# Optimization experiments

Hardware: AMD Instinct MI355X
Metric: run time of the kernel (lower is better)

Reference implementation:

```python
import jax, jax.numpy as jnp
import numpy as np

N_NODES = 100000
N_EDGES = 1_600_000
F_IN, HID, N_CLS = 128, 64, 32
NEG_SLOPE = 0.2  # PyG GATv2Conv default


def _segment_softmax(scores, seg, num_segments):
    # numerically stable softmax over edges grouped by destination node
    m = jax.ops.segment_max(scores, seg, num_segments=num_segments)
    ex = jnp.exp(scores - m[seg])
    s = jax.ops.segment_sum(ex, seg, num_segments=num_segments)
    return ex / (s[seg] + 1e-16)


def _gatv2_layer(x, src, dst, Wl, bl, Wr, br, att, bias, num_nodes):
    xl = x @ Wl + bl              # source transform  [N, C]
    xr = x @ Wr + br              # target transform  [N, C]
    # per-edge GATv2 attention logit: a . leaky_relu(xl_j + xr_i)
    e = jax.nn.leaky_relu(xl[src] + xr[dst], NEG_SLOPE) @ att  # [E]
    alpha = _segment_softmax(e, dst, num_nodes)                 # [E]
    out = jax.ops.segment_sum(alpha[:, None] * xl[src], dst, num_segments=num_nodes)
    return out + bias


def _add_self_loops(edge_index, n):
    loops = jnp.arange(n, dtype=edge_index.dtype)
    return jnp.concatenate([edge_index, jnp.stack([loops, loops])], axis=1)


def setup_inputs() -> dict:
    key = jax.random.key(0)
    ks = jax.random.split(key, 8)
    s1 = 1.0 / np.sqrt(F_IN)
    s2 = 1.0 / np.sqrt(HID)
    return {
        "x": jax.random.normal(ks[0], (N_NODES, F_IN), jnp.float32),
        "edge_index": jax.random.randint(ks[1], (2, N_EDGES), 0, N_NODES, jnp.int64),
        "W1l": jax.random.normal(ks[2], (F_IN, HID), jnp.float32) * s1,
        "b1l": jnp.zeros((HID,), jnp.float32),
        "W1r": jax.random.normal(ks[3], (F_IN, HID), jnp.float32) * s1,
        "b1r": jnp.zeros((HID,), jnp.float32),
        "att1": jax.random.normal(ks[4], (HID,), jnp.float32) * s2,
        "bias1": jnp.zeros((HID,), jnp.float32),
        "W2l": jax.random.normal(ks[5], (HID, N_CLS), jnp.float32) * s2,
        "b2l": jnp.zeros((N_CLS,), jnp.float32),
        "W2r": jax.random.normal(ks[6], (HID, N_CLS), jnp.float32) * s2,
        "b2r": jnp.zeros((N_CLS,), jnp.float32),
        "att2": jax.random.normal(ks[7], (N_CLS,), jnp.float32) / np.sqrt(N_CLS),
        "bias2": jnp.zeros((N_CLS,), jnp.float32),
    }


def reference(x, edge_index, W1l, b1l, W1r, b1r, att1, bias1,
              W2l, b2l, W2r, b2r, att2, bias2):
    n = x.shape[0]
    ei = _add_self_loops(edge_index, n)
    src, dst = ei[0], ei[1]
    h = jax.nn.relu(_gatv2_layer(x, src, dst, W1l, b1l, W1r, b1r, att1, bias1, n))
    # F.dropout(training=False) is identity in eval mode
    out = _gatv2_layer(h, src, dst, W2l, b2l, W2r, b2r, att2, bias2, n)
    return out
```

## Files before the change

### kernel.cpp

```cpp
#include <hip/hip_runtime.h>
#include <hip/hip_fp16.h>
#include <math.h>

#define F_IN 128
#define HID 64
#define NCLS 32
#define NEG 0.2f
#define NBKT 256
#define CHUNK 8192

using bf8 = __attribute__((ext_vector_type(8))) short;
using f4v = __attribute__((ext_vector_type(4))) float;
typedef _Float16 hv2 __attribute__((ext_vector_type(2)));

__device__ __forceinline__ void f4fma(float4& a, float s, const float4& w) {
    a.x = fmaf(s, w.x, a.x);
    a.y = fmaf(s, w.y, a.y);
    a.z = fmaf(s, w.z, a.z);
    a.w = fmaf(s, w.w, a.w);
}
__device__ __forceinline__ unsigned short f2bf(float f) {
    unsigned u = __float_as_uint(f);
    return (unsigned short)((u + 0x7FFFu + ((u >> 16) & 1u)) >> 16);
}
__device__ __forceinline__ unsigned short f2h(float f) {
    return __half_as_ushort(__float2half(f));
}
__device__ __forceinline__ float h2f(unsigned short u) {
    return __half2float(__ushort_as_half(u));
}
__device__ __forceinline__ unsigned pkaddabs(unsigned a, unsigned b) {
    hv2 r = __builtin_bit_cast(hv2, a) + __builtin_bit_cast(hv2, b);
    return __builtin_bit_cast(unsigned, r) & 0x7FFF7FFFu;
}
__device__ __forceinline__ float fdot2(unsigned a, unsigned b, float c) {
    return __builtin_amdgcn_fdot2(__builtin_bit_cast(hv2, a),
                                  __builtin_bit_cast(hv2, b), c, false);
}
__device__ __forceinline__ float h2lo(unsigned a) {
    return (float)__builtin_bit_cast(hv2, a).x;
}
__device__ __forceinline__ float h2hi(unsigned a) {
    return (float)__builtin_bit_cast(hv2, a).y;
}
template <int CTRL>
__device__ __forceinline__ float dpp_add(float v) {
    int t = __builtin_amdgcn_update_dpp(0, __float_as_int(v), CTRL, 0xf, 0xf, true);
    return v + __int_as_float(t);
}
__device__ __forceinline__ float swz16_add(float v) {
    int t = __builtin_amdgcn_ds_swizzle(__float_as_int(v), 0x401F);
    return v + __int_as_float(t);
}


__global__ __launch_bounds__(256) void zeroBuckets(int* __restrict__ bucketSize, int BK) {
    int i = blockIdx.x * 256 + threadIdx.x;
    if (i < BK) bucketSize[i] = 0;
}

__global__ __launch_bounds__(256) void bucketHist(const int* __restrict__ ei,
                                                  int Eorig, int Etot,
                                                  int* __restrict__ bucketSize, int BK) {
    __shared__ int h[512];
    int t = threadIdx.x;
    for (int j = t; j < BK; j += 256) h[j] = 0;
    __syncthreads();
    int base = blockIdx.x * CHUNK;
    int end = base + CHUNK < Etot ? base + CHUNK : Etot;
    for (int i = base + t; i < end; i += 256) {
        int dst = i < Eorig ? ei[Eorig + i] : i - Eorig;
        atomicAdd(&h[dst >> 8], 1);
    }
    __syncthreads();
    for (int j = t; j < BK; j += 256)
        if (h[j]) atomicAdd(&bucketSize[j], h[j]);
}

__global__ __launch_bounds__(256) void bucketScan(const int* __restrict__ bucketSize,
                                                  int* __restrict__ bucketStart,
                                                  int* __restrict__ bucketCursor,
                                                  int BK, int Etot) {
    __shared__ int sd[256];
    int t = threadIdx.x;
    int v0 = (2 * t     < BK) ? bucketSize[2 * t]     : 0;
    int v1 = (2 * t + 1 < BK) ? bucketSize[2 * t + 1] : 0;
    int ts = v0 + v1;
    sd[t] = ts;
    __syncthreads();
    for (int off = 1; off < 256; off <<= 1) {
        int x = (t >= off) ? sd[t - off] : 0;
        __syncthreads();
        sd[t] += x;
        __syncthreads();
    }
    int excl = sd[t] - ts;
    if (2 * t < BK)     { bucketStart[2 * t] = excl;          bucketCursor[2 * t] = excl; }
    if (2 * t + 1 < BK) { bucketStart[2 * t + 1] = excl + v0; bucketCursor[2 * t + 1] = excl + v0; }
    if (t == 255) bucketStart[BK] = Etot;
}

__global__ __launch_bounds__(256) void bucketScatter(const int* __restrict__ ei,
                                                     int Eorig, int Etot,
                                                     int* __restrict__ bucketCursor,
                                                     int* __restrict__ pairs, int BK) {
    __shared__ int h[512], lbase[512], hcur[512];
    int t = threadIdx.x;
    for (int j = t; j < BK; j += 256) { h[j] = 0; hcur[j] = 0; }
    __syncthreads();
    int base = blockIdx.x * CHUNK;
    int end = base + CHUNK < Etot ? base + CHUNK : Etot;
    for (int i = base + t; i < end; i += 256) {
        int dst = i < Eorig ? ei[Eorig + i] : i - Eorig;
        atomicAdd(&h[dst >> 8], 1);
    }
    __syncthreads();
    for (int j = t; j < BK; j += 256)
        lbase[j] = h[j] ? atomicAdd(&bucketCursor[j], h[j]) : 0;
    __syncthreads();
    for (int i = base + t; i < end; i += 256) {
        int src, dst;
        if (i < Eorig) { src = ei[i]; dst = ei[Eorig + i]; }
        else           { src = dst = i - Eorig; }
        int b = dst >> 8;
        int off = atomicAdd(&hcur[b], 1);
        pairs[lbase[b] + off] = (src << 8) | (dst & 255);
    }
}

__global__ __launch_bounds__(256) void bucketCSR(const int* __restrict__ pairs,
                                                 const int* __restrict__ bucketStart,
                                                 int* __restrict__ rowstart,
                                                 int* __restrict__ cnt,
                                                 int* __restrict__ srclist, int N) {
    __shared__ int c[256], cur[256];
    int t = threadIdx.x;
    int b = blockIdx.x;
    int lo = b * NBKT;
    int eb = bucketStart[b], ee = bucketStart[b + 1];
    c[t] = 0;
    __syncthreads();
    for (int i = eb + t; i < ee; i += 256)
        atomicAdd(&c[pairs[i] & 255], 1);
    __syncthreads();
    cur[t] = c[t];
    __syncthreads();
    for (int off = 1; off < 256; off <<= 1) {
        int x = (t >= off) ? cur[t - off] : 0;
        __syncthreads();
        cur[t] += x;
        __syncthreads();
    }
    int excl = cur[t] - c[t];
    int node = lo + t;
    if (node < N) { rowstart[node] = eb + excl; cnt[node] = c[t]; }
    __syncthreads();
    cur[t] = excl;
    __syncthreads();
    for (int i = eb + t; i < ee; i += 256) {
        int v = pairs[i];
        int pos = atomicAdd(&cur[v & 255], 1);
        srclist[eb + pos] = v >> 8;
    }
}

__global__ __launch_bounds__(256) void prepW(const float* __restrict__ Wl,
                                             const float* __restrict__ Wr,
                                             const float* __restrict__ att1,
                                             const float* __restrict__ att2,
                                             uint4* __restrict__ wfrag,
                                             unsigned short* __restrict__ att1h,
                                             unsigned short* __restrict__ att2h) {
    int e = blockIdx.x * 256 + threadIdx.x;
    if (e >= 2048) {
        int i = e - 2048;
        if (i < HID) att1h[i] = f2h(att1[i]);
        else if (i < HID + NCLS) att2h[i - HID] = f2h(att2[i - HID]);
        return;
    }
    int lane = e & 63;
    int kt = (e >> 6) & 3;
    int ct = (e >> 8) & 3;
    int mat = e >> 10;
    const float* W = mat ? Wr : Wl;
    int k0 = kt * 32 + (lane >> 4) * 8;
    int c = ct * 16 + (lane & 15);
    unsigned short h[8];
#pragma unroll
    for (int j = 0; j < 8; j++) h[j] = f2bf(W[(k0 + j) * HID + c]);
    wfrag[e] = *(uint4*)h;
}

__global__ __launch_bounds__(256) void transform1(const float* __restrict__ x,
                                                  const uint4* __restrict__ wfrag,
                                                  const float* __restrict__ bl,
                                                  const float* __restrict__ br,
                                                  const float* __restrict__ att,
                                                  unsigned short* __restrict__ xlh,
                                                  unsigned short* __restrict__ xrh,
                                                  float* __restrict__ sl, int N) {
    __shared__ uint4 sw[2048];
    int t = threadIdx.x;
#pragma unroll
    for (int j = 0; j < 8; j++) sw[t + j * 256] = wfrag[t + j * 256];
    __syncthreads();

    int w = t >> 6, lane = t & 63;
    int nb = blockIdx.x * 64 + w * 16;
    int m = lane & 15, quad = lane >> 4;

    int arow = nb + m; if (arow >= N) arow = N - 1;
    const float* xrow = x + (size_t)arow * F_IN + quad * 8;
    bf8 afr[4];
#pragma unroll
    for (int kt = 0; kt < 4; kt++) {
        float4 lo = *(const float4*)(xrow + kt * 32);
        float4 hi = *(const float4*)(xrow + kt * 32 + 4);
        unsigned short hh[8];
        hh[0] = f2bf(lo.x); hh[1] = f2bf(lo.y); hh[2] = f2bf(lo.z); hh[3] = f2bf(lo.w);
        hh[4] = f2bf(hi.x); hh[5] = f2bf(hi.y); hh[6] = f2bf(hi.z); hh[7] = f2bf(hi.w);
        afr[kt] = *(bf8*)hh;
    }

    float am[4];
#pragma unroll
    for (int ct = 0; ct < 4; ct++) am[ct] = att[ct * 16 + m];
    float slp[4] = {0.f, 0.f, 0.f, 0.f};

#pragma unroll
    for (int mat = 0; mat < 2; mat++) {
        const float* bias = mat ? br : bl;
#pragma unroll
        for (int ct = 0; ct < 4; ct++) {
            f4v acc = {0.f, 0.f, 0.f, 0.f};
#pragma unroll
            for (int kt = 0; kt < 4; kt++) {
                bf8 bfr = *(bf8*)&sw[((mat * 4 + ct) * 4 + kt) * 64 + lane];
                acc = __builtin_amdgcn_mfma_f32_16x16x32_bf16(afr[kt], bfr, acc, 0, 0, 0);
            }
            int ch = ct * 16 + m;
            float bv = bias[ch];
#pragma unroll
            for (int reg = 0; reg < 4; reg++) {
                int node = nb + quad * 4 + reg;
                float o = acc[reg] + bv;
                if (mat) {
                    if (node < N) xrh[(size_t)node * HID + ch] = f2h(o);
                } else {
                    unsigned short hb = f2h(o);
                    slp[reg] = fmaf(am[ct], h2f(hb), slp[reg]);
                    if (node < N) xlh[(size_t)node * HID + ch] = hb;
                }
            }
        }
    }
#pragma unroll
    for (int o2 = 1; o2 < 16; o2 <<= 1) {
#pragma unroll
        for (int reg = 0; reg < 4; reg++) slp[reg] += __shfl_xor(slp[reg], o2, 64);
    }
    if (m == 0) {
#pragma unroll
        for (int reg = 0; reg < 4; reg++) {
            int node = nb + quad * 4 + reg;
            if (node < N) sl[node] = 0.6f * slp[reg];
        }
    }
}

__global__ __launch_bounds__(256) void transform2(const float* __restrict__ h,
                                                  const float* __restrict__ Wl,
                                                  const float* __restrict__ bl,
                                                  const float* __restrict__ Wr,
                                                  const float* __restrict__ br,
                                                  const float* __restrict__ att,
                                                  unsigned short* __restrict__ xlh,
                                                  unsigned short* __restrict__ xrh,
                                                  float* __restrict__ sl, int N) {
    __shared__ float sWl[HID * NCLS];
    __shared__ float sWr[HID * NCLS];
    __shared__ float sx[128][68];
    int t = threadIdx.x;
    int nb = blockIdx.x * 128;

#pragma unroll
    for (int j = 0; j < 2; j++) {
        int f = t + j * 256;
        ((float4*)sWl)[f] = ((const float4*)Wl)[f];
        ((float4*)sWr)[f] = ((const float4*)Wr)[f];
    }
    int maxf = (N - nb) * 16;
#pragma unroll
    for (int j = 0; j < 8; j++) {
        int f = t + j * 256;
        int node = f >> 4, kc = f & 15;
        float4 v = {0.f, 0.f, 0.f, 0.f};
        if (f < maxf) v = ((const float4*)(h + (size_t)nb * HID))[f];
        v.x = fmaxf(v.x, 0.f);
        v.y = fmaxf(v.y, 0.f);
        v.z = fmaxf(v.z, 0.f);
        v.w = fmaxf(v.w, 0.f);
        *(float4*)&sx[node][kc * 4] = v;
    }
    __syncthreads();

    int c4 = (t & 7) * 4;
    int slot = t >> 3;
    float4 bl4 = *(const float4*)(bl + c4);
    float4 br4 = *(const float4*)(br + c4);
    float4 at4 = *(const float4*)(att + c4);
    float4 accl[4] = {bl4, bl4, bl4, bl4};
    float4 accr[4] = {br4, br4, br4, br4};

#pragma unroll 4
    for (int k4 = 0; k4 < HID / 4; k4++) {
        int k = k4 * 4;
        float4 wl0 = *(const float4*)&sWl[(k + 0) * NCLS + c4];
        float4 wl1 = *(const float4*)&sWl[(k + 1) * NCLS + c4];
        float4 wl2 = *(const float4*)&sWl[(k + 2) * NCLS + c4];
        float4 wl3 = *(const float4*)&sWl[(k + 3) * NCLS + c4];
        float4 wr0 = *(const float4*)&sWr[(k + 0) * NCLS + c4];
        float4 wr1 = *(const float4*)&sWr[(k + 1) * NCLS + c4];
        float4 wr2 = *(const float4*)&sWr[(k + 2) * NCLS + c4];
        float4 wr3 = *(const float4*)&sWr[(k + 3) * NCLS + c4];
#pragma unroll
        for (int j = 0; j < 4; j++) {
            float4 xv = *(const float4*)&sx[slot + j * 32][k];
            f4fma(accl[j], xv.x, wl0); f4fma(accr[j], xv.x, wr0);
            f4fma(accl[j], xv.y, wl1); f4fma(accr[j], xv.y, wr1);
            f4fma(accl[j], xv.z, wl2); f4fma(accr[j], xv.z, wr2);
            f4fma(accl[j], xv.w, wl3); f4fma(accr[j], xv.w, wr3);
        }
    }
#pragma unroll
    for (int j = 0; j < 4; j++) {
        ushort4 o;
        o.x = f2h(accl[j].x); o.y = f2h(accl[j].y);
        o.z = f2h(accl[j].z); o.w = f2h(accl[j].w);
        ushort4 orr;
        orr.x = f2h(accr[j].x); orr.y = f2h(accr[j].y);
        orr.z = f2h(accr[j].z); orr.w = f2h(accr[j].w);
        float slpj = fmaf(at4.x, h2f(o.x),
                     fmaf(at4.y, h2f(o.y),
                     fmaf(at4.z, h2f(o.z), at4.w * h2f(o.w))));
        slpj += __shfl_xor(slpj, 1, 64);
        slpj += __shfl_xor(slpj, 2, 64);
        slpj += __shfl_xor(slpj, 4, 64);
        int g = nb + slot + j * 32;
        if (g < N) {
            *(ushort4*)(xlh + (size_t)g * NCLS + c4) = o;
            *(ushort4*)(xrh + (size_t)g * NCLS + c4) = orr;
            if ((t & 7) == 0) sl[g] = 0.6f * slpj;
        }
    }
}

#define AGG_BATCH(EIDX, CLAMP, WEXPR)                                 \
    {                                                                 \
        int eidx = row + (EIDX);                                      \
        if (CLAMP) eidx = min(eidx, rowend1);                         \
        int src = srclist[eidx];                                      \
        float tA = sl[src];                                           \
        unsigned vp[NH];                                              \
        const unsigned short* rowp = xlh + (unsigned)src * C + cb0;   \
        if (NH == 4) *(uint4*)vp = *(const uint4*)rowp;               \
        else         *(uint2*)vp = *(const uint2*)rowp;               \
        float pa = 0.f;                                               \
        _Pragma("unroll")                                             \
        for (int j = 0; j < NH; j++)                                  \
            pa = fdot2(pkaddabs(vp[j], xrp[j]), atp[j], pa);          \
        pa = dpp_add<0x128>(pa);                                      \
        pa = swz16_add(pa);                                           \
        pa += __shfl_xor(pa, 32, 64);                                 \
        float wgt = (WEXPR);                                          \
        s += wgt;                                                     \
        _Pragma("unroll")                                             \
        for (int j = 0; j < NH; j++) {                                \
            acc[2 * j]     = fmaf(wgt, h2lo(vp[j]), acc[2 * j]);      \
            acc[2 * j + 1] = fmaf(wgt, h2hi(vp[j]), acc[2 * j + 1]);  \
        }                                                             \
    }

template <int C>
__global__ __launch_bounds__(256) void fusedAggE(const unsigned short* __restrict__ xlh,
                                                 const unsigned short* __restrict__ xrh,
                                                 const unsigned short* __restrict__ atth,
                                                 const float* __restrict__ sl,
                                                 const int* __restrict__ rowstart,
                                                 const int* __restrict__ cnt,
                                                 const int* __restrict__ srclist,
                                                 const float* __restrict__ bias,
                                                 float* __restrict__ out, int N) {
    constexpr int CH = C / 8;
    constexpr int NH = CH / 2;
    int wid = threadIdx.x >> 6;
    int lane = threadIdx.x & 63;
    int n = blockIdx.x * 4 + wid;
    if (n >= N) return;

    int slot = lane & 7;
    int pos  = lane >> 3;
    int cb0  = pos * CH;

    unsigned xrp[NH], atp[NH];
    if (NH == 4) {
        *(uint4*)xrp = *(const uint4*)(xrh + (size_t)n * C + cb0);
        *(uint4*)atp = *(const uint4*)(atth + cb0);
    } else {
        *(uint2*)xrp = *(const uint2*)(xrh + (size_t)n * C + cb0);
        *(uint2*)atp = *(const uint2*)(atth + cb0);
    }

    int row = rowstart[n];
    int deg = cnt[n];
    int rowend1 = row + deg - 1;

    float s = 0.f;
    float acc[CH];
#pragma unroll
    for (int c = 0; c < CH; c++) acc[c] = 0.f;

    for (int cb = 0; cb < deg; cb += 64) {
        int len = deg - cb; if (len > 64) len = 64;
        int nfull = len >> 3, rem = len & 7;
#pragma unroll 2
        for (int b = 0; b < nfull; b++) {
            AGG_BATCH(cb + b * 8 + slot, false, __expf(fmaf(0.4f, pa, tA)))
        }
        if (rem) {
            AGG_BATCH(cb + nfull * 8 + slot, true,
                      (slot < rem) ? __expf(fmaf(0.4f, pa, tA)) : 0.f)
        }
    }
#pragma unroll
    for (int c = 0; c < CH; c++) {
        acc[c] = dpp_add<0xB1>(acc[c]);
        acc[c] = dpp_add<0x4E>(acc[c]);
        acc[c] = dpp_add<0x141>(acc[c]);
    }
    s = dpp_add<0xB1>(s);
    s = dpp_add<0x4E>(s);
    s = dpp_add<0x141>(s);

    if (slot == 0) {
        float inv = 1.f / (s + 1e-16f);
        float o8[CH];
        float bi[CH];
        if (NH == 4) {
            *(float4*)&bi[0] = *(const float4*)(bias + cb0);
            *(float4*)&bi[4] = *(const float4*)(bias + cb0 + 4);
        } else {
            *(float4*)&bi[0] = *(const float4*)(bias + cb0);
        }
#pragma unroll
        for (int c = 0; c < CH; c++) o8[c] = fmaf(acc[c], inv, bi[c]);
        if (NH == 4) {
            *(float4*)(out + (size_t)n * C + cb0)     = *(float4*)&o8[0];
            *(float4*)(out + (size_t)n * C + cb0 + 4) = *(float4*)&o8[4];
        } else {
            *(float4*)(out + (size_t)n * C + cb0) = *(float4*)&o8[0];
        }
    }
}

extern "C" void kernel_launch(void* const* d_in, const int* in_sizes, int n_in,
                              void* d_out, int out_size, void* d_ws, size_t ws_size,
                              hipStream_t stream) {
    const float* x     = (const float*)d_in[0];
    const int*   ei    = (const int*)d_in[1];
    const float* W1l   = (const float*)d_in[2];
    const float* b1l   = (const float*)d_in[3];
    const float* W1r   = (const float*)d_in[4];
    const float* b1r   = (const float*)d_in[5];
    const float* att1  = (const float*)d_in[6];
    const float* bias1 = (const float*)d_in[7];
    const float* W2l   = (const float*)d_in[8];
    const float* b2l   = (const float*)d_in[9];
    const float* W2r   = (const float*)d_in[10];
    const float* b2r   = (const float*)d_in[11];
    const float* att2  = (const float*)d_in[12];
    const float* bias2 = (const float*)d_in[13];
    float* out = (float*)d_out;

    int N     = in_sizes[0] / F_IN;
    int Eorig = in_sizes[1] / 2;
    int Etot  = Eorig + N;
    int BK    = (N + NBKT - 1) / NBKT;

    char* p = (char*)d_ws;
    auto alloc = [&](size_t bytes) { void* r = (void*)p; p += (bytes + 255) & ~(size_t)255; return r; };
    unsigned short* xl1h = (unsigned short*)alloc((size_t)N * HID * 2);
    unsigned short* xr1h = (unsigned short*)alloc((size_t)N * HID * 2);
    float* h       = (float*)alloc((size_t)N * HID * 4);
    unsigned short* xl2h = (unsigned short*)alloc((size_t)N * NCLS * 2);
    unsigned short* xr2h = (unsigned short*)alloc((size_t)N * NCLS * 2);
    int*   cnt     = (int*)alloc((size_t)N * 4);
    int*   rowstart= (int*)alloc((size_t)N * 4);
    int*   srclist = (int*)alloc((size_t)Etot * 4);
    uint4* wfrag   = (uint4*)alloc(2048 * 16);
    float* sl1     = (float*)alloc((size_t)N * 4);
    float* sl2     = (float*)alloc((size_t)N * 4);
    unsigned short* att1h = (unsigned short*)alloc(HID * 2);
    unsigned short* att2h = (unsigned short*)alloc(NCLS * 2);
    int*   bucketSize   = (int*)alloc(520 * 4);
    int*   bucketStart  = (int*)alloc(520 * 4);
    int*   bucketCursor = (int*)alloc(520 * 4);
    int*   pairs   = (int*)h;

    int nChunks = (Etot + CHUNK - 1) / CHUNK;

    zeroBuckets<<<2, 256, 0, stream>>>(bucketSize, BK);
    bucketHist<<<nChunks, 256, 0, stream>>>(ei, Eorig, Etot, bucketSize, BK);
    bucketScan<<<1, 256, 0, stream>>>(bucketSize, bucketStart, bucketCursor, BK, Etot);
    bucketScatter<<<nChunks, 256, 0, stream>>>(ei, Eorig, Etot, bucketCursor, pairs, BK);
    bucketCSR<<<BK, 256, 0, stream>>>(pairs, bucketStart, rowstart, cnt, srclist, N);

    prepW<<<9, 256, 0, stream>>>(W1l, W1r, att1, att2, wfrag, att1h, att2h);
    transform1<<<(N + 63) / 64, 256, 0, stream>>>(x, wfrag, b1l, b1r, att1, xl1h, xr1h, sl1, N);
    fusedAggE<HID><<<(N + 3) / 4, 256, 0, stream>>>(xl1h, xr1h, att1h, sl1, rowstart, cnt,
                                                    srclist, bias1, h, N);

    transform2<<<(N + 127) / 128, 256, 0, stream>>>(h, W2l, b2l, W2r, b2r, att2, xl2h, xr2h, sl2, N);
    fusedAggE<NCLS><<<(N + 3) / 4, 256, 0, stream>>>(xl2h, xr2h, att2h, sl2, rowstart, cnt,
                                                     srclist, bias2, out, N);
}
```

Baseline: 319.6 us.

## Cooperatively load edge indices per wave and software-pipeline row gathers in aggregation

The aggregation kernel now loads up to 64 source indices and their per-node scalars once per wave with one coalesced load, and hands them to slots via shuffles instead of each slot reloading them per batch. The gather of the next batch's xl row is issued before the current batch's dot product and accumulation, overlapping memory latency with compute. The swizzle reduction is replaced by a shuffle-xor, and the bucket zeroing kernel becomes a memset. This adds register pressure from the double-buffered rows and extra cross-lane shuffles.

```diff
diff --git a/kernel.cpp b/kernel.cpp
--- a/kernel.cpp
+++ b/kernel.cpp
@@ -48,16 +48,7 @@
     int t = __builtin_amdgcn_update_dpp(0, __float_as_int(v), CTRL, 0xf, 0xf, true);
     return v + __int_as_float(t);
 }
-__device__ __forceinline__ float swz16_add(float v) {
-    int t = __builtin_amdgcn_ds_swizzle(__float_as_int(v), 0x401F);
-    return v + __int_as_float(t);
-}
-
-
-__global__ __launch_bounds__(256) void zeroBuckets(int* __restrict__ bucketSize, int BK) {
-    int i = blockIdx.x * 256 + threadIdx.x;
-    if (i < BK) bucketSize[i] = 0;
-}
+
 
 __global__ __launch_bounds__(256) void bucketHist(const int* __restrict__ ei,
                                                   int Eorig, int Etot,
@@ -355,34 +346,15 @@
     }
 }
 
-#define AGG_BATCH(EIDX, CLAMP, WEXPR)                                 \
-    {                                                                 \
-        int eidx = row + (EIDX);                                      \
-        if (CLAMP) eidx = min(eidx, rowend1);                         \
-        int src = srclist[eidx];                                      \
-        float tA = sl[src];                                           \
-        unsigned vp[NH];                                              \
-        const unsigned short* rowp = xlh + (unsigned)src * C + cb0;   \
-        if (NH == 4) *(uint4*)vp = *(const uint4*)rowp;               \
-        else         *(uint2*)vp = *(const uint2*)rowp;               \
-        float pa = 0.f;                                               \
-        _Pragma("unroll")                                             \
-        for (int j = 0; j < NH; j++)                                  \
-            pa = fdot2(pkaddabs(vp[j], xrp[j]), atp[j], pa);          \
-        pa = dpp_add<0x128>(pa);                                      \
-        pa = swz16_add(pa);                                           \
-        pa += __shfl_xor(pa, 32, 64);                                 \
-        float wgt = (WEXPR);                                          \
-        s += wgt;                                                     \
-        _Pragma("unroll")                                             \
-        for (int j = 0; j < NH; j++) {                                \
-            acc[2 * j]     = fmaf(wgt, h2lo(vp[j]), acc[2 * j]);      \
-            acc[2 * j + 1] = fmaf(wgt, h2hi(vp[j]), acc[2 * j + 1]);  \
-        }                                                             \
+#define LOADROW(VP, SRC)                                                  \
+    {                                                                     \
+        const unsigned short* rp = xlh + (unsigned)(SRC) * C + cb0;       \
+        if (NH == 4) *(uint4*)(VP) = *(const uint4*)rp;                   \
+        else         *(uint2*)(VP) = *(const uint2*)rp;                   \
     }
 
 template <int C>
-__global__ __launch_bounds__(256) void fusedAggE(const unsigned short* __restrict__ xlh,
+__global__ __launch_bounds__(256) void fusedAggF(const unsigned short* __restrict__ xlh,
                                                  const unsigned short* __restrict__ xrh,
                                                  const unsigned short* __restrict__ atth,
                                                  const float* __restrict__ sl,
@@ -413,7 +385,6 @@
 
     int row = rowstart[n];
     int deg = cnt[n];
-    int rowend1 = row + deg - 1;
 
     float s = 0.f;
     float acc[CH];
@@ -422,14 +393,47 @@
 
     for (int cb = 0; cb < deg; cb += 64) {
         int len = deg - cb; if (len > 64) len = 64;
-        int nfull = len >> 3, rem = len & 7;
-#pragma unroll 2
-        for (int b = 0; b < nfull; b++) {
-            AGG_BATCH(cb + b * 8 + slot, false, __expf(fmaf(0.4f, pa, tA)))
-        }
-        if (rem) {
-            AGG_BATCH(cb + nfull * 8 + slot, true,
-                      (slot < rem) ? __expf(fmaf(0.4f, pa, tA)) : 0.f)
+        int len1 = len - 1;
+        int li = lane < len ? lane : len1;
+        int srcv = srclist[row + cb + li];
+        float slv = sl[srcv];
+        int nbatch = (len + 7) >> 3;
+
+        int e0 = min(slot, len1);
+        float tA = __shfl(slv, e0, 64);
+        int srcA = __shfl(srcv, e0, 64);
+        unsigned vpA[NH];
+        LOADROW(vpA, srcA)
+
+        for (int b = 0; b < nbatch; b++) {
+            unsigned vpN[NH];
+            float tN = 0.f;
+            bool more = (b + 1 < nbatch);
+            if (more) {
+                int eN = min((b + 1) * 8 + slot, len1);
+                tN = __shfl(slv, eN, 64);
+                int srcN = __shfl(srcv, eN, 64);
+                LOADROW(vpN, srcN)
+            }
+            float pa = 0.f;
+#pragma unroll
+            for (int j = 0; j < NH; j++)
+                pa = fdot2(pkaddabs(vpA[j], xrp[j]), atp[j], pa);
+            pa = dpp_add<0x128>(pa);
+            pa += __shfl_xor(pa, 16, 64);
+            pa += __shfl_xor(pa, 32, 64);
+            float wgt = (b * 8 + slot < len) ? __expf(fmaf(0.4f, pa, tA)) : 0.f;
+            s += wgt;
+#pragma unroll
+            for (int j = 0; j < NH; j++) {
+                acc[2 * j]     = fmaf(wgt, h2lo(vpA[j]), acc[2 * j]);
+                acc[2 * j + 1] = fmaf(wgt, h2hi(vpA[j]), acc[2 * j + 1]);
+            }
+            if (more) {
+#pragma unroll
+                for (int j = 0; j < NH; j++) vpA[j] = vpN[j];
+                tA = tN;
+            }
         }
     }
 #pragma unroll
@@ -509,7 +513,7 @@
 
     int nChunks = (Etot + CHUNK - 1) / CHUNK;
 
-    zeroBuckets<<<2, 256, 0, stream>>>(bucketSize, BK);
+    hipMemsetAsync(bucketSize, 0, 520 * 4, stream);
     bucketHist<<<nChunks, 256, 0, stream>>>(ei, Eorig, Etot, bucketSize, BK);
     bucketScan<<<1, 256, 0, stream>>>(bucketSize, bucketStart, bucketCursor, BK, Etot);
     bucketScatter<<<nChunks, 256, 0, stream>>>(ei, Eorig, Etot, bucketCursor, pairs, BK);
@@ -517,10 +521,10 @@
 
     prepW<<<9, 256, 0, stream>>>(W1l, W1r, att1, att2, wfrag, att1h, att2h);
     transform1<<<(N + 63) / 64, 256, 0, stream>>>(x, wfrag, b1l, b1r, att1, xl1h, xr1h, sl1, N);
-    fusedAggE<HID><<<(N + 3) / 4, 256, 0, stream>>>(xl1h, xr1h, att1h, sl1, rowstart, cnt,
+    fusedAggF<HID><<<(N + 3) / 4, 256, 0, stream>>>(xl1h, xr1h, att1h, sl1, rowstart, cnt,
                                                     srclist, bias1, h, N);
 
     transform2<<<(N + 127) / 128, 256, 0, stream>>>(h, W2l, b2l, W2r, b2r, att2, xl2h, xr2h, sl2, N);
-    fusedAggE<NCLS><<<(N + 3) / 4, 256, 0, stream>>>(xl2h, xr2h, att2h, sl2, rowstart, cnt,
+    fusedAggF<NCLS><<<(N + 3) / 4, 256, 0, stream>>>(xl2h, xr2h, att2h, sl2, rowstart, cnt,
                                                      srclist, bias2, out, N);
 }
```

Result: faster. 302.7 us (-5.3%).
